# Optimization experiments

Hardware: AMD Instinct MI355X
Metric: run time of the kernel (lower is better)

## Reference

```python
import jax, jax.numpy as jnp
import numpy as np
import math

B, C_IN, C_OUT, K, STYLE_DIM, H, W = 16, 512, 512, 3, 512, 64, 64
EPS = 1e-8
CONV_SCALE = 1.0 / math.sqrt(C_IN * K * K)   # fan_in scale in ModulatedConv2d
MOD_SCALE = 1.0 / math.sqrt(STYLE_DIM)       # EqualLinear scale (lr_mul=1)


def setup_inputs() -> dict:
    key = jax.random.key(0)
    k1, k2, k3, k4 = jax.random.split(key, 4)
    inp = {
        "input": jax.random.normal(k1, (B, C_IN, H, W), dtype=jnp.float32),
        "style": jax.random.normal(k2, (B, STYLE_DIM), dtype=jnp.float32),
        # learned params
        "conv_weight": jax.random.normal(k3, (1, C_OUT, C_IN, K, K), dtype=jnp.float32),
        "mod_weight": jax.random.normal(k4, (C_IN, STYLE_DIM), dtype=jnp.float32),
        "mod_bias": jnp.ones((C_IN,), dtype=jnp.float32),  # bias_init=1
    }
    return inp


def reference(input, style, conv_weight, mod_weight, mod_bias):
    # EqualLinear modulation: style_mod[b, c_in]
    s = style @ (mod_weight * MOD_SCALE).T + mod_bias  # [B, C_in]
    # per-sample modulated weight: [B, C_out, C_in, K, K]
    w = CONV_SCALE * conv_weight * s[:, None, :, None, None]
    # demodulation
    demod = jax.lax.rsqrt(jnp.sum(w * w, axis=(2, 3, 4)) + EPS)  # [B, C_out]
    w = w * demod[:, :, None, None, None]
    # per-sample conv2d with 'same' padding (pad = K // 2), equivalent to groups=batch
    pad = K // 2

    def conv_one(x, wk):
        # x: [C_in, H, W], wk: [C_out, C_in, K, K]
        return jax.lax.conv_general_dilated(
            x[None], wk, window_strides=(1, 1),
            padding=[(pad, pad), (pad, pad)],
            dimension_numbers=("NCHW", "OIHW", "NCHW"))[0]

    out = jax.vmap(conv_one)(input, w)  # [B, C_out, H, W]
    return out
```

## Files before the change

### kernel.cpp

```cpp
#include <hip/hip_runtime.h>
#include <cstdint>
#include <cstddef>

#define BATCH 16
#define CIN 512
#define COUT 512
#define STYLE_D 512
#define EPSC 1e-8f
#define CONV_SCALE_F 0.014731391274719739f
#define MOD_SCALE_F  0.04419417382415922f

typedef __attribute__((ext_vector_type(8))) short bhalf8;
typedef __attribute__((ext_vector_type(16))) float f32x16;

__device__ __forceinline__ unsigned short f2bf(float f){
  unsigned int u = __float_as_uint(f);
  u += 0x7fffu + ((u >> 16) & 1u);
  return (unsigned short)(u >> 16);
}

__device__ __forceinline__ void load_lds16(const void* g, void* l){
  __builtin_amdgcn_global_load_lds(
      (const __attribute__((address_space(1))) uint32_t*)g,
      (__attribute__((address_space(3))) uint32_t*)l, 16, 0, 0);
}

__global__ void k_style(const float* __restrict__ style, const float* __restrict__ mw,
                        const float* __restrict__ mb, float* __restrict__ a){
  int t = blockIdx.x * 256 + threadIdx.x;
  int b = t >> 9, c = t & 511;
  const float4* s4 = (const float4*)(style + b * STYLE_D);
  const float4* w4 = (const float4*)(mw + (size_t)c * STYLE_D);
  float s = 0.f;
#pragma unroll 4
  for (int k = 0; k < STYLE_D / 4; ++k){
    float4 sv = s4[k], wv = w4[k];
    s += sv.x * wv.x + sv.y * wv.y + sv.z * wv.z + sv.w * wv.w;
  }
  s = s * MOD_SCALE_F + mb[c];
  a[t] = CONV_SCALE_F * s;
}

__global__ void k_wprep(const float* __restrict__ cw, float* __restrict__ r,
                        unsigned short* __restrict__ W2){
  int t = blockIdx.x * 256 + threadIdx.x;
  int co = t >> 9, ci = t & 511;
  const float* w = cw + (size_t)t * 9;
  float acc = 0.f; float v[9];
#pragma unroll
  for (int j = 0; j < 9; ++j){ v[j] = w[j]; acc += v[j] * v[j]; }
  r[t] = acc;
#pragma unroll
  for (int tap = 0; tap < 9; ++tap)
    W2[((size_t)tap * COUT + co) * CIN + ci] = f2bf(v[tap]);
}

__global__ void k_demod(const float* __restrict__ a, const float* __restrict__ r,
                        float* __restrict__ d){
  int t = blockIdx.x * 256 + threadIdx.x;
  int b = t >> 9, co = t & 511;
  const float4* a4 = (const float4*)(a + b * CIN);
  const float4* r4 = (const float4*)(r + (size_t)co * CIN);
  float s = 0.f;
#pragma unroll 4
  for (int k = 0; k < CIN / 4; ++k){
    float4 av = a4[k], rv = r4[k];
    s += av.x*av.x*rv.x + av.y*av.y*rv.y + av.z*av.z*rv.z + av.w*av.w*rv.w;
  }
  d[t] = rsqrtf(s + EPSC);
}

__global__ __launch_bounds__(256) void k_xprep(const float* __restrict__ in,
                                               const float* __restrict__ a,
                                               unsigned short* __restrict__ x2){
  __shared__ float tile[64][67];
  int bx = blockIdx.x;
  int b = bx >> 9, cgrp = (bx >> 6) & 7, y = bx & 63;
  int c0 = cgrp * 64;
  int tid = threadIdx.x;
  int xx = tid & 63, c4 = tid >> 6;
  const float* src = in + ((size_t)(b * CIN + c0)) * 4096 + y * 64;
#pragma unroll
  for (int i = 0; i < 16; ++i){
    int cl = i * 4 + c4;
    tile[cl][xx] = src[(size_t)cl * 4096 + xx];
  }
  __syncthreads();
  int cg = tid & 31;
  float a0 = a[b * CIN + c0 + cg * 2];
  float a1 = a[b * CIN + c0 + cg * 2 + 1];
  unsigned int* dst = (unsigned int*)(x2 + ((size_t)(b * 4096 + y * 64)) * CIN + c0);
#pragma unroll
  for (int i = 0; i < 8; ++i){
    int px = i * 8 + (tid >> 5);
    float v0 = tile[cg * 2][px], v1 = tile[cg * 2 + 1][px];
    unsigned int pack = (unsigned int)f2bf(a0 * v0) | ((unsigned int)f2bf(a1 * v1) << 16);
    dst[(size_t)px * (CIN / 2) + cg] = pack;
  }
}

#define LDS_W_BASE 19584
#define NCHUNK_TOT 2376
__global__ __launch_bounds__(256, 2) void k_conv(
    const unsigned short* __restrict__ x2, const unsigned short* __restrict__ W2,
    const float* __restrict__ dmod, const char* __restrict__ zp,
    float* __restrict__ out){
  __shared__ __align__(16) unsigned char smem[2560 * 16];

  int bx = blockIdx.x;
  int b = bx >> 6, coT = (bx >> 3) & 7, pt = bx & 7;
  int y0 = (pt >> 1) * 16, x0 = (pt & 1) * 32;
  int tid = threadIdx.x, lane = tid & 63, w = tid >> 6;

  const char* ga[10];
#pragma unroll
  for (int i = 0; i < 10; ++i){
    int chunk = i * 256 + tid;
    const char* p;
    if (chunk < 1224){
      int pix = chunk >> 1, kh = chunk & 1;
      int iy = pix / 34, ix = pix - iy * 34;
      int gy = y0 + iy - 1, gx = x0 + ix - 1;
      if (gy >= 0 && gy < 64 && gx >= 0 && gx < 64)
        p = (const char*)x2 + (((size_t)(b * 4096 + gy * 64 + gx)) * CIN + kh * 8) * 2;
      else p = zp;
    } else if (chunk < NCHUNK_TOT){
      int sw = chunk - 1224;
      int tap = sw >> 7, cf = (sw >> 6) & 1, kh = (sw >> 5) & 1, co = sw & 31;
      p = (const char*)W2 + (((size_t)(tap * COUT + coT * 64 + cf * 32 + co)) * CIN + kh * 8) * 2;
    } else {
      p = zp;
    }
    ga[i] = p;
  }

  f32x16 acc[2][4];
#pragma unroll
  for (int cf = 0; cf < 2; ++cf)
#pragma unroll
    for (int nf = 0; nf < 4; ++nf)
#pragma unroll
      for (int e = 0; e < 16; ++e) acc[cf][nf][e] = 0.f;

  const unsigned bvLane = (unsigned)((lane & 31) * 32 + (lane >> 5) * 16);
  const unsigned char* wbase = smem + LDS_W_BASE + lane * 16;
  const unsigned wrow = (unsigned)(w * 4);

  for (int s = 0; s < 32; ++s){
#pragma unroll
    for (int i = 0; i < 10; ++i){
      load_lds16(ga[i], smem + (i * 256 + tid) * 16);
      ga[i] += 32;
    }
    __syncthreads();
#pragma unroll
    for (int tap = 0; tap < 9; ++tap){
      const int ki = tap / 3, kj = tap - ki * 3;
      bhalf8 a0 = *(const bhalf8*)(wbase + tap * 2048);
      bhalf8 a1 = *(const bhalf8*)(wbase + tap * 2048 + 1024);
#pragma unroll
      for (int nf = 0; nf < 4; ++nf){
        bhalf8 bv = *(const bhalf8*)(smem + ((wrow + nf + ki) * 34 + kj) * 32 + bvLane);
        acc[0][nf] = __builtin_amdgcn_mfma_f32_32x32x16_bf16(a0, bv, acc[0][nf], 0, 0, 0);
        acc[1][nf] = __builtin_amdgcn_mfma_f32_32x32x16_bf16(a1, bv, acc[1][nf], 0, 0, 0);
      }
    }
    __syncthreads();
  }

  int n = lane & 31, kh = lane >> 5;
  const float* dp = dmod + b * COUT + coT * 64;
#pragma unroll
  for (int cf = 0; cf < 2; ++cf){
#pragma unroll
    for (int nf = 0; nf < 4; ++nf){
      int gy = y0 + w * 4 + nf;
      float* orow = out + ((size_t)(b * COUT + coT * 64 + cf * 32)) * 4096 + gy * 64 + x0 + n;
#pragma unroll
      for (int reg = 0; reg < 16; ++reg){
        int row = (reg & 3) + 8 * (reg >> 2) + 4 * kh;
        orow[(size_t)row * 4096] = dp[cf * 32 + row] * acc[cf][nf][reg];
      }
    }
  }
}

__global__ void k_demod_direct(const float* __restrict__ a, const float* __restrict__ cw,
                               float* __restrict__ d){
  int t = blockIdx.x * 256 + threadIdx.x;
  int b = t & 15, co = t >> 4;
  const float* ar = a + b * CIN;
  const float* wr = cw + (size_t)co * CIN * 9;
  float s = 0.f;
  for (int ci = 0; ci < CIN; ++ci){
    float av = ar[ci], rr = 0.f;
#pragma unroll
    for (int j = 0; j < 9; ++j){ float v = wr[ci * 9 + j]; rr += v * v; }
    s += av * av * rr;
  }
  d[b * COUT + co] = rsqrtf(s + EPSC);
}

__global__ void k_conv_naive(const float* __restrict__ in, const float* __restrict__ cw,
                             const float* __restrict__ a, const float* __restrict__ d,
                             float* __restrict__ out){
  size_t t = (size_t)blockIdx.x * 256 + threadIdx.x;
  int x = t & 63, y = (t >> 6) & 63;
  int co = (t >> 12) & 511, b = (int)(t >> 21);
  const float* ar = a + b * CIN;
  const float* wr = cw + (size_t)co * CIN * 9;
  const float* ib = in + (size_t)b * CIN * 4096;
  float acc = 0.f;
  for (int ci = 0; ci < CIN; ++ci){
    float av = ar[ci];
    const float* ip = ib + (size_t)ci * 4096;
    const float* wp = wr + ci * 9;
#pragma unroll
    for (int dy = 0; dy < 3; ++dy){
      int gy = y + dy - 1;
      if (gy < 0 || gy > 63) continue;
#pragma unroll
      for (int dx = 0; dx < 3; ++dx){
        int gx = x + dx - 1;
        if (gx < 0 || gx > 63) continue;
        acc += wp[dy * 3 + dx] * av * ip[gy * 64 + gx];
      }
    }
  }
  out[t] = d[b * COUT + co] * acc;
}

extern "C" void kernel_launch(void* const* d_in, const int* in_sizes, int n_in,
                              void* d_out, int out_size, void* d_ws, size_t ws_size,
                              hipStream_t stream){
  (void)in_sizes; (void)n_in; (void)out_size;
  const float* in    = (const float*)d_in[0];
  const float* style = (const float*)d_in[1];
  const float* cw    = (const float*)d_in[2];
  const float* mw    = (const float*)d_in[3];
  const float* mb    = (const float*)d_in[4];
  float* out = (float*)d_out;

  char* ws = (char*)d_ws;
  const size_t ZP_OFF = 0;
  const size_t A_OFF  = 4096;
  const size_t D_OFF  = A_OFF + 32768;
  const size_t R_OFF  = D_OFF + 32768;
  const size_t W2_OFF = R_OFF + 1048576;
  const size_t X2_OFF = W2_OFF + (size_t)9 * COUT * CIN * 2;
  const size_t WS_NEED = X2_OFF + (size_t)BATCH * 4096 * CIN * 2;

  float* a    = (float*)(ws + A_OFF);
  float* dmod = (float*)(ws + D_OFF);

  if (ws_size >= WS_NEED){
    float* r = (float*)(ws + R_OFF);
    unsigned short* W2 = (unsigned short*)(ws + W2_OFF);
    unsigned short* x2 = (unsigned short*)(ws + X2_OFF);
    hipMemsetAsync(ws + ZP_OFF, 0, 4096, stream);
    k_style<<<32, 256, 0, stream>>>(style, mw, mb, a);
    k_wprep<<<1024, 256, 0, stream>>>(cw, r, W2);
    k_demod<<<32, 256, 0, stream>>>(a, r, dmod);
    k_xprep<<<8192, 256, 0, stream>>>(in, a, x2);
    k_conv<<<1024, 256, 0, stream>>>(x2, W2, dmod, ws + ZP_OFF, out);
  } else {
    k_style<<<32, 256, 0, stream>>>(style, mw, mb, a);
    k_demod_direct<<<32, 256, 0, stream>>>(a, cw, dmod);
    k_conv_naive<<<131072, 256, 0, stream>>>(in, cw, a, dmod, out);
  }
}
```

Baseline: 527.7 us.

## Double-buffer conv LDS loads, reuse B fragments across taps, merge prep kernels

```diff
diff --git a/kernel.cpp b/kernel.cpp
--- a/kernel.cpp
+++ b/kernel.cpp
@@ -25,113 +25,117 @@
       (__attribute__((address_space(3))) uint32_t*)l, 16, 0, 0);
 }
 
-__global__ void k_style(const float* __restrict__ style, const float* __restrict__ mw,
-                        const float* __restrict__ mb, float* __restrict__ a){
-  int t = blockIdx.x * 256 + threadIdx.x;
-  int b = t >> 9, c = t & 511;
-  const float4* s4 = (const float4*)(style + b * STYLE_D);
-  const float4* w4 = (const float4*)(mw + (size_t)c * STYLE_D);
-  float s = 0.f;
+__global__ __launch_bounds__(256) void k_prep1(
+    const float* __restrict__ style, const float* __restrict__ mw,
+    const float* __restrict__ mb, const float* __restrict__ cw,
+    float* __restrict__ a, float* __restrict__ r, unsigned short* __restrict__ W2){
+  int bx = blockIdx.x;
+  if (bx < 32){
+    int t = bx * 256 + threadIdx.x;
+    int b = t >> 9, c = t & 511;
+    const float4* s4 = (const float4*)(style + b * STYLE_D);
+    const float4* w4 = (const float4*)(mw + (size_t)c * STYLE_D);
+    float s = 0.f;
 #pragma unroll 4
-  for (int k = 0; k < STYLE_D / 4; ++k){
-    float4 sv = s4[k], wv = w4[k];
-    s += sv.x * wv.x + sv.y * wv.y + sv.z * wv.z + sv.w * wv.w;
-  }
-  s = s * MOD_SCALE_F + mb[c];
-  a[t] = CONV_SCALE_F * s;
-}
-
-__global__ void k_wprep(const float* __restrict__ cw, float* __restrict__ r,
-                        unsigned short* __restrict__ W2){
-  int t = blockIdx.x * 256 + threadIdx.x;
-  int co = t >> 9, ci = t & 511;
-  const float* w = cw + (size_t)t * 9;
-  float acc = 0.f; float v[9];
-#pragma unroll
-  for (int j = 0; j < 9; ++j){ v[j] = w[j]; acc += v[j] * v[j]; }
-  r[t] = acc;
-#pragma unroll
-  for (int tap = 0; tap < 9; ++tap)
-    W2[((size_t)tap * COUT + co) * CIN + ci] = f2bf(v[tap]);
-}
-
-__global__ void k_demod(const float* __restrict__ a, const float* __restrict__ r,
-                        float* __restrict__ d){
-  int t = blockIdx.x * 256 + threadIdx.x;
-  int b = t >> 9, co = t & 511;
-  const float4* a4 = (const float4*)(a + b * CIN);
-  const float4* r4 = (const float4*)(r + (size_t)co * CIN);
-  float s = 0.f;
-#pragma unroll 4
-  for (int k = 0; k < CIN / 4; ++k){
-    float4 av = a4[k], rv = r4[k];
-    s += av.x*av.x*rv.x + av.y*av.y*rv.y + av.z*av.z*rv.z + av.w*av.w*rv.w;
-  }
-  d[t] = rsqrtf(s + EPSC);
-}
-
-__global__ __launch_bounds__(256) void k_xprep(const float* __restrict__ in,
-                                               const float* __restrict__ a,
-                                               unsigned short* __restrict__ x2){
+    for (int k = 0; k < STYLE_D / 4; ++k){
+      float4 sv = s4[k], wv = w4[k];
+      s += sv.x * wv.x + sv.y * wv.y + sv.z * wv.z + sv.w * wv.w;
+    }
+    s = s * MOD_SCALE_F + mb[c];
+    a[t] = CONV_SCALE_F * s;
+  } else {
+    int t = (bx - 32) * 256 + threadIdx.x;
+    int co = t >> 9, ci = t & 511;
+    const float* w = cw + (size_t)t * 9;
+    float acc = 0.f; float v[9];
+#pragma unroll
+    for (int j = 0; j < 9; ++j){ v[j] = w[j]; acc += v[j] * v[j]; }
+    r[t] = acc;
+#pragma unroll
+    for (int tap = 0; tap < 9; ++tap)
+      W2[((size_t)tap * COUT + co) * CIN + ci] = f2bf(v[tap]);
+  }
+}
+
+__global__ __launch_bounds__(256) void k_prep2(
+    const float* __restrict__ in, const float* __restrict__ a,
+    const float* __restrict__ r, unsigned short* __restrict__ x2,
+    float* __restrict__ d){
   __shared__ float tile[64][67];
   int bx = blockIdx.x;
-  int b = bx >> 9, cgrp = (bx >> 6) & 7, y = bx & 63;
-  int c0 = cgrp * 64;
-  int tid = threadIdx.x;
-  int xx = tid & 63, c4 = tid >> 6;
-  const float* src = in + ((size_t)(b * CIN + c0)) * 4096 + y * 64;
-#pragma unroll
-  for (int i = 0; i < 16; ++i){
-    int cl = i * 4 + c4;
-    tile[cl][xx] = src[(size_t)cl * 4096 + xx];
-  }
-  __syncthreads();
-  int cg = tid & 31;
-  float a0 = a[b * CIN + c0 + cg * 2];
-  float a1 = a[b * CIN + c0 + cg * 2 + 1];
-  unsigned int* dst = (unsigned int*)(x2 + ((size_t)(b * 4096 + y * 64)) * CIN + c0);
-#pragma unroll
-  for (int i = 0; i < 8; ++i){
-    int px = i * 8 + (tid >> 5);
-    float v0 = tile[cg * 2][px], v1 = tile[cg * 2 + 1][px];
-    unsigned int pack = (unsigned int)f2bf(a0 * v0) | ((unsigned int)f2bf(a1 * v1) << 16);
-    dst[(size_t)px * (CIN / 2) + cg] = pack;
-  }
-}
-
-#define LDS_W_BASE 19584
-#define NCHUNK_TOT 2376
+  if (bx < 8192){
+    int b = bx >> 9, cgrp = (bx >> 6) & 7, y = bx & 63;
+    int c0 = cgrp * 64;
+    int tid = threadIdx.x;
+    int xx = tid & 63, c4 = tid >> 6;
+    const float* src = in + ((size_t)(b * CIN + c0)) * 4096 + y * 64;
+#pragma unroll
+    for (int i = 0; i < 16; ++i){
+      int cl = i * 4 + c4;
+      tile[cl][xx] = src[(size_t)cl * 4096 + xx];
+    }
+    __syncthreads();
+    int cg = tid & 31;
+    float a0 = a[b * CIN + c0 + cg * 2];
+    float a1 = a[b * CIN + c0 + cg * 2 + 1];
+    unsigned int* dst = (unsigned int*)(x2 + ((size_t)(b * 4096 + y * 64)) * CIN + c0);
+#pragma unroll
+    for (int i = 0; i < 8; ++i){
+      int px = i * 8 + (tid >> 5);
+      float v0 = tile[cg * 2][px], v1 = tile[cg * 2 + 1][px];
+      unsigned int pack = (unsigned int)f2bf(a0 * v0) | ((unsigned int)f2bf(a1 * v1) << 16);
+      dst[(size_t)px * (CIN / 2) + cg] = pack;
+    }
+  } else {
+    int t = (bx - 8192) * 256 + threadIdx.x;
+    int b = t >> 9, co = t & 511;
+    const float4* a4 = (const float4*)(a + b * CIN);
+    const float4* r4 = (const float4*)(r + (size_t)co * CIN);
+    float s = 0.f;
+#pragma unroll 4
+    for (int k = 0; k < CIN / 4; ++k){
+      float4 av = a4[k], rv = r4[k];
+      s += av.x*av.x*rv.x + av.y*av.y*rv.y + av.z*av.z*rv.z + av.w*av.w*rv.w;
+    }
+    d[t] = rsqrtf(s + EPSC);
+  }
+}
+
+#define BUFSZ 39936
+#define W_LDS_OFF 19584
 __global__ __launch_bounds__(256, 2) void k_conv(
-    const unsigned short* __restrict__ x2, const unsigned short* __restrict__ W2,
-    const float* __restrict__ dmod, const char* __restrict__ zp,
-    float* __restrict__ out){
-  __shared__ __align__(16) unsigned char smem[2560 * 16];
+    const char* __restrict__ ws, const float* __restrict__ dmod,
+    float* __restrict__ out,
+    unsigned int x2_off, unsigned int w2_off){
+  __shared__ __align__(16) unsigned char smem[2 * BUFSZ];
 
   int bx = blockIdx.x;
   int b = bx >> 6, coT = (bx >> 3) & 7, pt = bx & 7;
   int y0 = (pt >> 1) * 16, x0 = (pt & 1) * 32;
   int tid = threadIdx.x, lane = tid & 63, w = tid >> 6;
 
-  const char* ga[10];
+  unsigned int off[10], dst_off[10];
 #pragma unroll
   for (int i = 0; i < 10; ++i){
     int chunk = i * 256 + tid;
-    const char* p;
+    int slot = (chunk < 2432) ? chunk : (2432 + (chunk & 63));
+    dst_off[i] = (unsigned)slot * 16u;
+    unsigned int o;
     if (chunk < 1224){
       int pix = chunk >> 1, kh = chunk & 1;
       int iy = pix / 34, ix = pix - iy * 34;
       int gy = y0 + iy - 1, gx = x0 + ix - 1;
       if (gy >= 0 && gy < 64 && gx >= 0 && gx < 64)
-        p = (const char*)x2 + (((size_t)(b * 4096 + gy * 64 + gx)) * CIN + kh * 8) * 2;
-      else p = zp;
-    } else if (chunk < NCHUNK_TOT){
+        o = x2_off + (unsigned)(((b * 4096 + gy * 64 + gx) * CIN + kh * 8) * 2);
+      else o = 0;
+    } else if (chunk < 2376){
       int sw = chunk - 1224;
       int tap = sw >> 7, cf = (sw >> 6) & 1, kh = (sw >> 5) & 1, co = sw & 31;
-      p = (const char*)W2 + (((size_t)(tap * COUT + coT * 64 + cf * 32 + co)) * CIN + kh * 8) * 2;
+      o = w2_off + (unsigned)(((tap * COUT + coT * 64 + cf * 32 + co) * CIN + kh * 8) * 2);
     } else {
-      p = zp;
-    }
-    ga[i] = p;
+      o = 0;
+    }
+    off[i] = o;
   }
 
   f32x16 acc[2][4];
@@ -143,29 +147,47 @@
       for (int e = 0; e < 16; ++e) acc[cf][nf][e] = 0.f;
 
   const unsigned bvLane = (unsigned)((lane & 31) * 32 + (lane >> 5) * 16);
-  const unsigned char* wbase = smem + LDS_W_BASE + lane * 16;
-  const unsigned wrow = (unsigned)(w * 4);
-
+  const unsigned aLane  = (unsigned)(W_LDS_OFF + lane * 16);
+  const unsigned wrow   = (unsigned)(w * 4);
+
+#pragma unroll
+  for (int i = 0; i < 10; ++i){
+    load_lds16(ws + off[i], smem + dst_off[i]);
+    off[i] += 32;
+  }
+  __syncthreads();
+
+  unsigned pbase = 0;
   for (int s = 0; s < 32; ++s){
-#pragma unroll
-    for (int i = 0; i < 10; ++i){
-      load_lds16(ga[i], smem + (i * 256 + tid) * 16);
-      ga[i] += 32;
+    unsigned pnext = pbase ^ BUFSZ;
+    if (s < 31){
+#pragma unroll
+      for (int i = 0; i < 10; ++i){
+        load_lds16(ws + off[i], smem + pnext + dst_off[i]);
+        off[i] += 32;
+      }
+    }
+    const unsigned char* buf = smem + pbase;
+#pragma unroll
+    for (int kj = 0; kj < 3; ++kj){
+      bhalf8 bv[6];
+#pragma unroll
+      for (int rr = 0; rr < 6; ++rr)
+        bv[rr] = *(const bhalf8*)(buf + ((wrow + rr) * 34 + kj) * 32 + bvLane);
+#pragma unroll
+      for (int ki = 0; ki < 3; ++ki){
+        int tap = ki * 3 + kj;
+        bhalf8 a0 = *(const bhalf8*)(buf + aLane + tap * 2048);
+        bhalf8 a1 = *(const bhalf8*)(buf + aLane + tap * 2048 + 1024);
+#pragma unroll
+        for (int nf = 0; nf < 4; ++nf){
+          acc[0][nf] = __builtin_amdgcn_mfma_f32_32x32x16_bf16(a0, bv[nf + ki], acc[0][nf], 0, 0, 0);
+          acc[1][nf] = __builtin_amdgcn_mfma_f32_32x32x16_bf16(a1, bv[nf + ki], acc[1][nf], 0, 0, 0);
+        }
+      }
     }
     __syncthreads();
-#pragma unroll
-    for (int tap = 0; tap < 9; ++tap){
-      const int ki = tap / 3, kj = tap - ki * 3;
-      bhalf8 a0 = *(const bhalf8*)(wbase + tap * 2048);
-      bhalf8 a1 = *(const bhalf8*)(wbase + tap * 2048 + 1024);
-#pragma unroll
-      for (int nf = 0; nf < 4; ++nf){
-        bhalf8 bv = *(const bhalf8*)(smem + ((wrow + nf + ki) * 34 + kj) * 32 + bvLane);
-        acc[0][nf] = __builtin_amdgcn_mfma_f32_32x32x16_bf16(a0, bv, acc[0][nf], 0, 0, 0);
-        acc[1][nf] = __builtin_amdgcn_mfma_f32_32x32x16_bf16(a1, bv, acc[1][nf], 0, 0, 0);
-      }
-    }
-    __syncthreads();
+    pbase = pnext;
   }
 
   int n = lane & 31, kh = lane >> 5;
@@ -183,6 +205,17 @@
       }
     }
   }
+}
+
+__global__ void k_style_f(const float* __restrict__ style, const float* __restrict__ mw,
+                          const float* __restrict__ mb, float* __restrict__ a){
+  int t = blockIdx.x * 256 + threadIdx.x;
+  int b = t >> 9, c = t & 511;
+  const float* s = style + b * STYLE_D;
+  const float* wv = mw + (size_t)c * STYLE_D;
+  float acc = 0.f;
+  for (int k = 0; k < STYLE_D; ++k) acc += s[k] * wv[k];
+  a[t] = CONV_SCALE_F * (acc * MOD_SCALE_F + mb[c]);
 }
 
 __global__ void k_demod_direct(const float* __restrict__ a, const float* __restrict__ cw,
@@ -258,13 +291,12 @@
     unsigned short* W2 = (unsigned short*)(ws + W2_OFF);
     unsigned short* x2 = (unsigned short*)(ws + X2_OFF);
     hipMemsetAsync(ws + ZP_OFF, 0, 4096, stream);
-    k_style<<<32, 256, 0, stream>>>(style, mw, mb, a);
-    k_wprep<<<1024, 256, 0, stream>>>(cw, r, W2);
-    k_demod<<<32, 256, 0, stream>>>(a, r, dmod);
-    k_xprep<<<8192, 256, 0, stream>>>(in, a, x2);
-    k_conv<<<1024, 256, 0, stream>>>(x2, W2, dmod, ws + ZP_OFF, out);
+    k_prep1<<<1056, 256, 0, stream>>>(style, mw, mb, cw, a, r, W2);
+    k_prep2<<<8224, 256, 0, stream>>>(in, a, r, x2, dmod);
+    k_conv<<<1024, 256, 0, stream>>>(ws, dmod, out,
+                                     (unsigned int)X2_OFF, (unsigned int)W2_OFF);
   } else {
-    k_style<<<32, 256, 0, stream>>>(style, mw, mb, a);
+    k_style_f<<<32, 256, 0, stream>>>(style, mw, mb, a);
     k_demod_direct<<<32, 256, 0, stream>>>(a, cw, dmod);
     k_conv_naive<<<131072, 256, 0, stream>>>(in, cw, a, dmod, out);
   }
```

Result: faster. 512.8 us (-2.8%).
